# Kernel tuning notes

Hardware: AMD Instinct MI355X
Metric: run time of the kernel (lower is better)

## Reference

```python
import jax, jax.numpy as jnp
import numpy as np

B, L, D_IN, D_OUT = 4, 2048, 4096, 4096


def setup_inputs() -> dict:
    key = jax.random.key(0)
    k1, k2, k3, k4 = jax.random.split(key, 4)
    x = jax.random.normal(k1, (B, L, D_IN), dtype=jnp.float32)
    # base weight stored transposed as [in, out], like self.base = base.T
    base = jax.random.normal(k2, (D_IN, D_OUT), dtype=jnp.float32) * 0.02
    # binary delta sign mask in {0, 1}, stored transposed [in, out]
    mask = jax.random.randint(k3, (D_IN, D_OUT), 0, 2).astype(jnp.int32)
    # coeff = mean(|finetune - base|); a small positive scalar
    coeff = jax.random.uniform(k4, (1,), dtype=jnp.float32) * 0.01
    return {"x": x, "base": base, "coeff": coeff, "mask": mask}


def reference(x, base, coeff, mask):
    # Original: x @ base.T_stored + coeff * (x @ repeated_mask)
    # (t_coeff * x) @ mask == t_coeff * (x @ mask); we avoid materializing the
    # per-batch repeated mask since broadcasting the [in, out] mask is equivalent.
    m = mask.astype(x.dtype)            # {0,1} dequantized mask, [in, out]
    c = coeff[0].astype(x.dtype)
    return jnp.einsum('bld,de->ble', x, base) + c * jnp.einsum('bld,de->ble', x, m)
```

## Files before the change

### kernel.cpp

```cpp
#include <hip/hip_runtime.h>
#include <hip/hip_bf16.h>
#include <stdint.h>

#define DIN 4096
#define DOUT 4096
#define BK 64
#define NT (DIN / BK)

typedef __attribute__((ext_vector_type(8))) short short8;
typedef __attribute__((ext_vector_type(8))) unsigned short ushort8;
typedef __attribute__((ext_vector_type(16))) float f32x16;

__device__ inline unsigned short f2bf(float f) {
    union { float f; unsigned u; } v; v.f = f;
    unsigned r = v.u + 0x7fffu + ((v.u >> 16) & 1u);
    return (unsigned short)(r >> 16);
}

__global__ void cvt_x_kernel(const float* __restrict__ x, ushort* __restrict__ xb, long n8) {
    long i = (long)blockIdx.x * blockDim.x + threadIdx.x;
    if (i >= n8) return;
    const float4* p = (const float4*)(x + i * 8);
    float4 v0 = p[0], v1 = p[1];
    ushort8 o;
    o[0] = f2bf(v0.x); o[1] = f2bf(v0.y); o[2] = f2bf(v0.z); o[3] = f2bf(v0.w);
    o[4] = f2bf(v1.x); o[5] = f2bf(v1.y); o[6] = f2bf(v1.z); o[7] = f2bf(v1.w);
    *(ushort8*)(xb + i * 8) = o;
}

__global__ void make_wt_kernel(const float* __restrict__ base, const int* __restrict__ mask,
                               const float* __restrict__ coeff, ushort* __restrict__ wt) {
    __shared__ float tile[64][65];
    const float c = coeff[0];
    const int t = threadIdx.x;
    const int bd = blockIdx.x >> 6;
    const int be = blockIdx.x & 63;
    const int d0 = bd * 64, e0 = be * 64;
#pragma unroll
    for (int i = 0; i < 4; ++i) {
        int idx = i * 256 + t;
        int r = idx >> 4;
        int c4 = (idx & 15) << 2;
        const float4 bv = *(const float4*)(base + (size_t)(d0 + r) * DOUT + e0 + c4);
        const int4  mv = *(const int4*)(mask + (size_t)(d0 + r) * DOUT + e0 + c4);
        tile[r][c4 + 0] = bv.x + c * (float)mv.x;
        tile[r][c4 + 1] = bv.y + c * (float)mv.y;
        tile[r][c4 + 2] = bv.z + c * (float)mv.z;
        tile[r][c4 + 3] = bv.w + c * (float)mv.w;
    }
    __syncthreads();
#pragma unroll
    for (int i = 0; i < 8; ++i) {
        int idx = i * 256 + t;
        int r = idx >> 5;
        int p = (idx & 31) << 1;
        ushort2 o;
        o.x = f2bf(tile[p][r]);
        o.y = f2bf(tile[p + 1][r]);
        *(ushort2*)(wt + (size_t)(e0 + r) * DIN + d0 + p) = o;
    }
}


#define MFMA32(D, VA, VB) D = __builtin_amdgcn_mfma_f32_32x32x16_bf16(VA, VB, D, 0, 0, 0)

#define GLL(P, L) \
    __builtin_amdgcn_global_load_lds( \
        (const __attribute__((address_space(1))) void*)(P), \
        (__attribute__((address_space(3))) void*)(L), 16, 0, 0)

#define RDA(BUF,KK,MM,KC) (*(const short8*)&lA[BUF][KK][aoffA + (MM)*1024 + (KC)])
#define RDB(BUF,KK,NN,KC) (*(const short8*)&lB[BUF][KK][boffB + (NN)*1024 + (KC)])

#define STAGE_A(BUF,KK,OFE) { GLL(gA0 + (OFE), &lA[BUF][KK][doff]); \
                              GLL(gA1 + (OFE), &lA[BUF][KK][doff + 4096]); }
#define STAGE_B(BUF,KK,OFE) { GLL(gB0 + (OFE), &lB[BUF][KK][doff]); \
                              GLL(gB1 + (OFE), &lB[BUF][KK][doff + 4096]); }

#define WAITV(N)  asm volatile("s_waitcnt vmcnt(" #N ")" ::: "memory")
#define SBAR      __builtin_amdgcn_s_barrier()

#define MFMA_HALF(C0,C1,C2,C3) \
    MFMA32(C0, a0, b0); MFMA32(C1, a0, b2); MFMA32(C2, a1, b0); MFMA32(C3, a1, b2); \
    MFMA32(C0, a2, b1); MFMA32(C1, a2, b3); MFMA32(C2, a3, b1); MFMA32(C3, a3, b3);

#define KTILE(BUF, G1, G2, NEXT, OFE1, OFE2) \
  { \
    short8 a0,a1,a2,a3,b0,b1,b2,b3; \
     \
    a0=RDA(BUF,0,0,kc0); a2=RDA(BUF,0,0,kc1); a1=RDA(BUF,0,1,kc0); a3=RDA(BUF,0,1,kc1); \
    b0=RDB(BUF,0,0,kc0); b1=RDB(BUF,0,0,kc1); b2=RDB(BUF,0,1,kc0); b3=RDB(BUF,0,1,kc1); \
    if (G1) STAGE_A(1-(BUF), 1, OFE1) \
    SBAR; \
    __builtin_amdgcn_s_setprio(1); \
    MFMA_HALF(c0,c1,c2,c3) \
    __builtin_amdgcn_s_setprio(0); \
    WAITV(6); \
     \
    a0=RDA(BUF,0,2,kc0); a2=RDA(BUF,0,2,kc1); a1=RDA(BUF,0,3,kc0); a3=RDA(BUF,0,3,kc1); \
    if (G1) STAGE_B(1-(BUF), 1, OFE1) \
    SBAR; \
    __builtin_amdgcn_s_setprio(1); \
    MFMA_HALF(c4,c5,c6,c7) \
    __builtin_amdgcn_s_setprio(0); \
     \
    a0=RDA(BUF,1,0,kc0); a2=RDA(BUF,1,0,kc1); a1=RDA(BUF,1,1,kc0); a3=RDA(BUF,1,1,kc1); \
    b0=RDB(BUF,1,0,kc0); b1=RDB(BUF,1,0,kc1); b2=RDB(BUF,1,1,kc0); b3=RDB(BUF,1,1,kc1); \
    if (G2) STAGE_A(BUF, 0, OFE2) \
    SBAR; \
    __builtin_amdgcn_s_setprio(1); \
    MFMA_HALF(c0,c1,c2,c3) \
    __builtin_amdgcn_s_setprio(0); \
     \
    a0=RDA(BUF,1,2,kc0); a2=RDA(BUF,1,2,kc1); a1=RDA(BUF,1,3,kc0); a3=RDA(BUF,1,3,kc1); \
    if (G2) STAGE_B(BUF, 0, OFE2) \
    SBAR; \
    __builtin_amdgcn_s_setprio(1); \
    MFMA_HALF(c4,c5,c6,c7) \
    __builtin_amdgcn_s_setprio(0); \
    if (G2)        { WAITV(6); } \
    else if (NEXT) { WAITV(0); } \
    SBAR; \
    __builtin_amdgcn_sched_barrier(0); \
  }

__global__ __launch_bounds__(512, 2) void gemm_kernel(const ushort* __restrict__ A,
                                                      const ushort* __restrict__ Bt,
                                                      float* __restrict__ C) {
    __shared__ __align__(16) ushort lA[2][2][256 * 32];
    __shared__ __align__(16) ushort lB[2][2][256 * 32];

    const int tid = threadIdx.x;
    const int lane = tid & 63;
    const int wave = tid >> 6;

    const int nbn = DOUT / 256;
    const int nwg = gridDim.x;
    int bid = blockIdx.x;
    int cpx = nwg >> 3;
    int s = (bid & 7) * cpx + (bid >> 3);
    const int m0 = (s / nbn) * 256;
    const int n0 = (s % nbn) * 256;

    const int wr = wave >> 2;
    const int wc = wave & 3;
    const int fr = lane & 31;
    const int fq = lane >> 5;

    const int st_r = tid >> 2;

    const int sxe = ((fr >> 1) & 3) << 3;
    const int sxe8 = sxe & 8, sx16 = sxe & 16;
    const int kc0 = sx16;
    const int kc1 = 16 ^ sx16;
    const int aoffA = fr * 32 + ((fq << 3) ^ sxe8);
    const int aoffA2 = (wr * 128 + fr) * 32 + ((fq << 3) ^ sxe8);
    const int boffB = (wc * 64 + fr) * 32 + ((fq << 3) ^ sxe8);
    #define aoffA aoffA2

    const int doff = tid * 8;
    const int sce = ((tid & 3) << 3) ^ (((st_r >> 1) & 3) << 3);
    const ushort* gA0 = A  + (size_t)(m0 + st_r) * DIN + sce;
    const ushort* gA1 = gA0 + (size_t)128 * DIN;
    const ushort* gB0 = Bt + (size_t)(n0 + st_r) * DIN + sce;
    const ushort* gB1 = gB0 + (size_t)128 * DIN;

    f32x16 c0 = {}, c1 = {}, c2 = {}, c3 = {}, c4 = {}, c5 = {}, c6 = {}, c7 = {};

    STAGE_A(0, 0, 0)   STAGE_B(0, 0, 0)
    STAGE_A(0, 1, 32)  STAGE_B(0, 1, 32)
    STAGE_A(1, 0, 64)  STAGE_B(1, 0, 64)
    WAITV(6);
    SBAR;
    __builtin_amdgcn_sched_barrier(0);

    for (int u = 0; u < NT; u += 2) {
        KTILE(0, 1, (u + 2 < NT), 1, 96, 128)
        KTILE(1, (u + 2 < NT), (u + 3 < NT), (u + 2 < NT), 160, 192)
        gA0 += 128; gA1 += 128; gB0 += 128; gB1 += 128;
    }

    const int gcb = n0 + wc * 64 + fr;
    const int grb = m0 + wr * 128 + fq * 4;
#define WRT(CT, M32, N32) \
    _Pragma("unroll") \
    for (int r = 0; r < 16; ++r) { \
        int grow = grb + (M32) * 32 + (r & 3) + 8 * (r >> 2); \
        C[(size_t)grow * DOUT + gcb + (N32) * 32] = CT[r]; \
    }
    WRT(c0, 0, 0) WRT(c1, 0, 1) WRT(c2, 1, 0) WRT(c3, 1, 1)
    WRT(c4, 2, 0) WRT(c5, 2, 1) WRT(c6, 3, 0) WRT(c7, 3, 1)
#undef WRT
}

extern "C" void kernel_launch(void* const* d_in, const int* in_sizes, int n_in,
                              void* d_out, int out_size, void* d_ws, size_t ws_size,
                              hipStream_t stream) {
    const float* x = (const float*)d_in[0];
    const float* base = (const float*)d_in[1];
    const float* coeff = (const float*)d_in[2];
    const int* mask = (const int*)d_in[3];
    float* out = (float*)d_out;

    const int M = in_sizes[0] / DIN;
    ushort* xb = (ushort*)d_ws;
    ushort* wt = xb + (size_t)M * DIN;

    long n8 = (long)M * DIN / 8;
    cvt_x_kernel<<<(int)((n8 + 255) / 256), 256, 0, stream>>>(x, xb, n8);
    make_wt_kernel<<<(DIN / 64) * (DOUT / 64), 256, 0, stream>>>(base, mask, coeff, wt);

    const int nwg = (M / 256) * (DOUT / 256);
    gemm_kernel<<<nwg, 512, 0, stream>>>(xb, wt, out);
}
```

Before: 333.7 us.

## Pre-block A and B operands into tile-contiguous layout for GEMM loads

The activation conversion and weight preparation now write bf16 operands in a blocked layout: each 256-row by 64-K tile is contiguous and arranged to match the LDS fragment order. The GEMM's global-to-LDS loads become fully contiguous, and the XOR swizzle address math is replaced by fixed offsets. Weight reblocking adds an extra pass that uses the output buffer as scratch for the row-major weights. The intent is better load coalescing and simpler LDS reads, at the cost of one more kernel launch and an extra copy of the weight matrix, and the new LDS read pattern may introduce bank conflicts.

```diff
diff --git a/kernel.cpp b/kernel.cpp
--- a/kernel.cpp
+++ b/kernel.cpp
@@ -17,15 +17,25 @@
     return (unsigned short)(r >> 16);
 }
 
-__global__ void cvt_x_kernel(const float* __restrict__ x, ushort* __restrict__ xb, long n8) {
-    long i = (long)blockIdx.x * blockDim.x + threadIdx.x;
-    if (i >= n8) return;
-    const float4* p = (const float4*)(x + i * 8);
-    float4 v0 = p[0], v1 = p[1];
-    ushort8 o;
-    o[0] = f2bf(v0.x); o[1] = f2bf(v0.y); o[2] = f2bf(v0.z); o[3] = f2bf(v0.w);
-    o[4] = f2bf(v1.x); o[5] = f2bf(v1.y); o[6] = f2bf(v1.z); o[7] = f2bf(v1.w);
-    *(ushort8*)(xb + i * 8) = o;
+
+__global__ void cvt_x_blocked(const float* __restrict__ x, ushort* __restrict__ xb) {
+    const int t = threadIdx.x;
+    const int bx = blockIdx.x;
+    const int R = bx >> 6, u = bx & 63;
+    const int r32 = t >> 3, kcol = t & 7;
+    const int kk = kcol >> 2, s = (kcol >> 1) & 1, h = kcol & 1;
+    const float* src = x + ((size_t)R * 256) * DIN + u * 64 + kcol * 8;
+    ushort* dst = xb + (size_t)R * 1048576 + (size_t)u * 16384
+                + (size_t)kk * 8192 + s * 512 + r32 * 16 + h * 8;
+#pragma unroll
+    for (int j = 0; j < 8; ++j) {
+        const float* p = src + ((size_t)(j * 32 + r32)) * DIN;
+        float4 v0 = *(const float4*)p, v1 = *(const float4*)(p + 4);
+        ushort8 o;
+        o[0] = f2bf(v0.x); o[1] = f2bf(v0.y); o[2] = f2bf(v0.z); o[3] = f2bf(v0.w);
+        o[4] = f2bf(v1.x); o[5] = f2bf(v1.y); o[6] = f2bf(v1.z); o[7] = f2bf(v1.w);
+        *(ushort8*)(dst + (size_t)j * 1024) = o;
+    }
 }
 
 __global__ void make_wt_kernel(const float* __restrict__ base, const int* __restrict__ mask,
@@ -61,6 +71,22 @@
     }
 }
 
+__global__ void reblock_w(const ushort* __restrict__ wt_rm, ushort* __restrict__ wb) {
+    const int t = threadIdx.x;
+    const int bx = blockIdx.x;
+    const int R = bx >> 6, u = bx & 63;
+    const int r32 = t >> 3, kcol = t & 7;
+    const int kk = kcol >> 2, s = (kcol >> 1) & 1, h = kcol & 1;
+    const ushort* src = wt_rm + ((size_t)R * 256) * DIN + u * 64 + kcol * 8;
+    ushort* dst = wb + (size_t)R * 1048576 + (size_t)u * 16384
+                + (size_t)kk * 8192 + s * 512 + r32 * 16 + h * 8;
+#pragma unroll
+    for (int j = 0; j < 8; ++j) {
+        ushort8 o = *(const ushort8*)(src + ((size_t)(j * 32 + r32)) * DIN);
+        *(ushort8*)(dst + (size_t)j * 1024) = o;
+    }
+}
+
 
 #define MFMA32(D, VA, VB) D = __builtin_amdgcn_mfma_f32_32x32x16_bf16(VA, VB, D, 0, 0, 0)
 
@@ -69,8 +95,8 @@
         (const __attribute__((address_space(1))) void*)(P), \
         (__attribute__((address_space(3))) void*)(L), 16, 0, 0)
 
-#define RDA(BUF,KK,MM,KC) (*(const short8*)&lA[BUF][KK][aoffA + (MM)*1024 + (KC)])
-#define RDB(BUF,KK,NN,KC) (*(const short8*)&lB[BUF][KK][boffB + (NN)*1024 + (KC)])
+#define RDA(BUF,KK,MT,S) (*(const short8*)&lA[BUF][KK][awoff + (MT)*1024 + (S)*512])
+#define RDB(BUF,KK,NN,S) (*(const short8*)&lB[BUF][KK][bwoff + (NN)*1024 + (S)*512])
 
 #define STAGE_A(BUF,KK,OFE) { GLL(gA0 + (OFE), &lA[BUF][KK][doff]); \
                               GLL(gA1 + (OFE), &lA[BUF][KK][doff + 4096]); }
@@ -80,43 +106,41 @@
 #define WAITV(N)  asm volatile("s_waitcnt vmcnt(" #N ")" ::: "memory")
 #define SBAR      __builtin_amdgcn_s_barrier()
 
-#define MFMA_HALF(C0,C1,C2,C3) \
-    MFMA32(C0, a0, b0); MFMA32(C1, a0, b2); MFMA32(C2, a1, b0); MFMA32(C3, a1, b2); \
-    MFMA32(C0, a2, b1); MFMA32(C1, a2, b3); MFMA32(C2, a3, b1); MFMA32(C3, a3, b3);
+#define MFMA8(CX0,CX1,CY0,CY1) \
+    MFMA32(CX0, a0s0, b0s0); MFMA32(CX1, a0s0, b1s0); \
+    MFMA32(CY0, a1s0, b0s0); MFMA32(CY1, a1s0, b1s0); \
+    MFMA32(CX0, a0s1, b0s1); MFMA32(CX1, a0s1, b1s1); \
+    MFMA32(CY0, a1s1, b0s1); MFMA32(CY1, a1s1, b1s1);
 
 #define KTILE(BUF, G1, G2, NEXT, OFE1, OFE2) \
   { \
-    short8 a0,a1,a2,a3,b0,b1,b2,b3; \
-     \
-    a0=RDA(BUF,0,0,kc0); a2=RDA(BUF,0,0,kc1); a1=RDA(BUF,0,1,kc0); a3=RDA(BUF,0,1,kc1); \
-    b0=RDB(BUF,0,0,kc0); b1=RDB(BUF,0,0,kc1); b2=RDB(BUF,0,1,kc0); b3=RDB(BUF,0,1,kc1); \
+    short8 a0s0,a0s1,a1s0,a1s1,b0s0,b0s1,b1s0,b1s1; \
+    a0s0=RDA(BUF,0,0,0); a0s1=RDA(BUF,0,0,1); a1s0=RDA(BUF,0,1,0); a1s1=RDA(BUF,0,1,1); \
+    b0s0=RDB(BUF,0,0,0); b0s1=RDB(BUF,0,0,1); b1s0=RDB(BUF,0,1,0); b1s1=RDB(BUF,0,1,1); \
     if (G1) STAGE_A(1-(BUF), 1, OFE1) \
     SBAR; \
     __builtin_amdgcn_s_setprio(1); \
-    MFMA_HALF(c0,c1,c2,c3) \
+    MFMA8(c00,c01,c10,c11) \
     __builtin_amdgcn_s_setprio(0); \
     WAITV(6); \
-     \
-    a0=RDA(BUF,0,2,kc0); a2=RDA(BUF,0,2,kc1); a1=RDA(BUF,0,3,kc0); a3=RDA(BUF,0,3,kc1); \
+    a0s0=RDA(BUF,0,2,0); a0s1=RDA(BUF,0,2,1); a1s0=RDA(BUF,0,3,0); a1s1=RDA(BUF,0,3,1); \
     if (G1) STAGE_B(1-(BUF), 1, OFE1) \
     SBAR; \
     __builtin_amdgcn_s_setprio(1); \
-    MFMA_HALF(c4,c5,c6,c7) \
-    __builtin_amdgcn_s_setprio(0); \
-     \
-    a0=RDA(BUF,1,0,kc0); a2=RDA(BUF,1,0,kc1); a1=RDA(BUF,1,1,kc0); a3=RDA(BUF,1,1,kc1); \
-    b0=RDB(BUF,1,0,kc0); b1=RDB(BUF,1,0,kc1); b2=RDB(BUF,1,1,kc0); b3=RDB(BUF,1,1,kc1); \
+    MFMA8(c20,c21,c30,c31) \
+    __builtin_amdgcn_s_setprio(0); \
+    a0s0=RDA(BUF,1,0,0); a0s1=RDA(BUF,1,0,1); a1s0=RDA(BUF,1,1,0); a1s1=RDA(BUF,1,1,1); \
+    b0s0=RDB(BUF,1,0,0); b0s1=RDB(BUF,1,0,1); b1s0=RDB(BUF,1,1,0); b1s1=RDB(BUF,1,1,1); \
     if (G2) STAGE_A(BUF, 0, OFE2) \
     SBAR; \
     __builtin_amdgcn_s_setprio(1); \
-    MFMA_HALF(c0,c1,c2,c3) \
-    __builtin_amdgcn_s_setprio(0); \
-     \
-    a0=RDA(BUF,1,2,kc0); a2=RDA(BUF,1,2,kc1); a1=RDA(BUF,1,3,kc0); a3=RDA(BUF,1,3,kc1); \
+    MFMA8(c00,c01,c10,c11) \
+    __builtin_amdgcn_s_setprio(0); \
+    a0s0=RDA(BUF,1,2,0); a0s1=RDA(BUF,1,2,1); a1s0=RDA(BUF,1,3,0); a1s1=RDA(BUF,1,3,1); \
     if (G2) STAGE_B(BUF, 0, OFE2) \
     SBAR; \
     __builtin_amdgcn_s_setprio(1); \
-    MFMA_HALF(c4,c5,c6,c7) \
+    MFMA8(c20,c21,c30,c31) \
     __builtin_amdgcn_s_setprio(0); \
     if (G2)        { WAITV(6); } \
     else if (NEXT) { WAITV(0); } \
@@ -147,37 +171,31 @@
     const int fr = lane & 31;
     const int fq = lane >> 5;
 
-    const int st_r = tid >> 2;
-
-    const int sxe = ((fr >> 1) & 3) << 3;
-    const int sxe8 = sxe & 8, sx16 = sxe & 16;
-    const int kc0 = sx16;
-    const int kc1 = 16 ^ sx16;
-    const int aoffA = fr * 32 + ((fq << 3) ^ sxe8);
-    const int aoffA2 = (wr * 128 + fr) * 32 + ((fq << 3) ^ sxe8);
-    const int boffB = (wc * 64 + fr) * 32 + ((fq << 3) ^ sxe8);
-    #define aoffA aoffA2
-
+    const int awoff = wr * 4096 + fr * 16 + fq * 8;
+    const int bwoff = wc * 2048 + fr * 16 + fq * 8;
     const int doff = tid * 8;
-    const int sce = ((tid & 3) << 3) ^ (((st_r >> 1) & 3) << 3);
-    const ushort* gA0 = A  + (size_t)(m0 + st_r) * DIN + sce;
-    const ushort* gA1 = gA0 + (size_t)128 * DIN;
-    const ushort* gB0 = Bt + (size_t)(n0 + st_r) * DIN + sce;
-    const ushort* gB1 = gB0 + (size_t)128 * DIN;
-
-    f32x16 c0 = {}, c1 = {}, c2 = {}, c3 = {}, c4 = {}, c5 = {}, c6 = {}, c7 = {};
-
-    STAGE_A(0, 0, 0)   STAGE_B(0, 0, 0)
-    STAGE_A(0, 1, 32)  STAGE_B(0, 1, 32)
-    STAGE_A(1, 0, 64)  STAGE_B(1, 0, 64)
+
+    const ushort* Ablk = A  + (size_t)(m0 >> 8) * 1048576;
+    const ushort* Bblk = Bt + (size_t)(n0 >> 8) * 1048576;
+    const ushort* gA0 = Ablk + doff;
+    const ushort* gA1 = Ablk + doff + 4096;
+    const ushort* gB0 = Bblk + doff;
+    const ushort* gB1 = Bblk + doff + 4096;
+
+    f32x16 c00 = {}, c01 = {}, c10 = {}, c11 = {};
+    f32x16 c20 = {}, c21 = {}, c30 = {}, c31 = {};
+
+    STAGE_A(0, 0, 0)      STAGE_B(0, 0, 0)
+    STAGE_A(0, 1, 8192)   STAGE_B(0, 1, 8192)
+    STAGE_A(1, 0, 16384)  STAGE_B(1, 0, 16384)
     WAITV(6);
     SBAR;
     __builtin_amdgcn_sched_barrier(0);
 
     for (int u = 0; u < NT; u += 2) {
-        KTILE(0, 1, (u + 2 < NT), 1, 96, 128)
-        KTILE(1, (u + 2 < NT), (u + 3 < NT), (u + 2 < NT), 160, 192)
-        gA0 += 128; gA1 += 128; gB0 += 128; gB1 += 128;
+        KTILE(0, 1, (u + 2 < NT), 1, 24576, 32768)
+        KTILE(1, (u + 2 < NT), (u + 3 < NT), (u + 2 < NT), 40960, 49152)
+        gA0 += 32768; gA1 += 32768; gB0 += 32768; gB1 += 32768;
     }
 
     const int gcb = n0 + wc * 64 + fr;
@@ -188,8 +206,8 @@
         int grow = grb + (M32) * 32 + (r & 3) + 8 * (r >> 2); \
         C[(size_t)grow * DOUT + gcb + (N32) * 32] = CT[r]; \
     }
-    WRT(c0, 0, 0) WRT(c1, 0, 1) WRT(c2, 1, 0) WRT(c3, 1, 1)
-    WRT(c4, 2, 0) WRT(c5, 2, 1) WRT(c6, 3, 0) WRT(c7, 3, 1)
+    WRT(c00, 0, 0) WRT(c01, 0, 1) WRT(c10, 1, 0) WRT(c11, 1, 1)
+    WRT(c20, 2, 0) WRT(c21, 2, 1) WRT(c30, 3, 0) WRT(c31, 3, 1)
 #undef WRT
 }
 
@@ -204,12 +222,13 @@
 
     const int M = in_sizes[0] / DIN;
     ushort* xb = (ushort*)d_ws;
-    ushort* wt = xb + (size_t)M * DIN;
-
-    long n8 = (long)M * DIN / 8;
-    cvt_x_kernel<<<(int)((n8 + 255) / 256), 256, 0, stream>>>(x, xb, n8);
-    make_wt_kernel<<<(DIN / 64) * (DOUT / 64), 256, 0, stream>>>(base, mask, coeff, wt);
+    ushort* wb = xb + (size_t)M * DIN;
+    ushort* wt_rm = (ushort*)d_out;
+
+    cvt_x_blocked<<<(M / 256) * 64, 256, 0, stream>>>(x, xb);
+    make_wt_kernel<<<(DIN / 64) * (DOUT / 64), 256, 0, stream>>>(base, mask, coeff, wt_rm);
+    reblock_w<<<(DOUT / 256) * 64, 256, 0, stream>>>(wt_rm, wb);
 
     const int nwg = (M / 256) * (DOUT / 256);
-    gemm_kernel<<<nwg, 512, 0, stream>>>(xb, wt, out);
-}
+    gemm_kernel<<<nwg, 512, 0, stream>>>(xb, wb, out);
+}
```

Result: slower. 341.9 us (+2.5%).
